# Kernel tuning notes

Hardware: AMD Instinct MI355X
Metric: run time of the kernel (lower is better)

The kernel has to match this reference:

```python
import jax, jax.numpy as jnp
import numpy as np

N_HEADS = 16  # cfg.n_heads
ROPE_BASE = 10000.0


def _rope_sin_cos(T, head_dim, dtype):
    # standard NeoX-style rotary tables, shape (T, head_dim)
    inv_freq = 1.0 / (ROPE_BASE ** (jnp.arange(0, head_dim, 2, dtype=jnp.float32) / head_dim))
    freqs = jnp.arange(T, dtype=jnp.float32)[:, None] * inv_freq[None, :]  # (T, hd/2)
    emb = jnp.concatenate([freqs, freqs], axis=-1)                          # (T, hd)
    return jnp.sin(emb).astype(dtype), jnp.cos(emb).astype(dtype)


def _rotate_half(x):
    x1, x2 = jnp.split(x, 2, axis=-1)
    return jnp.concatenate([-x2, x1], axis=-1)


def setup_inputs() -> dict:
    key = jax.random.key(0)
    kx, kq, kp, kl = jax.random.split(key, 4)
    B, T, D = 4, 2048, 2048
    x = jax.random.normal(kx, (B, T, D), dtype=jnp.float32)
    # torch Linear weights: (out_features, in_features), no bias
    Wqkv = jax.random.normal(kq, (3 * D, D), dtype=jnp.float32) * (D ** -0.5)
    Wproj = jax.random.normal(kp, (D, D), dtype=jnp.float32) * (D ** -0.5)
    # padding at the end: valid lengths in [T//2, T]
    lengths = jax.random.randint(kl, (B,), T // 2, T + 1)
    attention_mask = (jnp.arange(T)[None, :] < lengths[:, None]).astype(jnp.int32)
    return {"x": x, "Wqkv": Wqkv, "Wproj": Wproj, "attention_mask": attention_mask}


def reference(x, Wqkv, Wproj, attention_mask):
    B, T, D = x.shape
    H = N_HEADS
    hd = D // H
    qkv = (x @ Wqkv.T).reshape(B, T, 3, H, hd)            # (B,T,3,H,hd)
    q, k, v = (jnp.moveaxis(qkv[:, :, i], 1, 2) for i in range(3))  # each (B,H,T,hd)
    sin, cos = _rope_sin_cos(T, hd, x.dtype)              # (T,hd), broadcast over B,H
    q = q * cos + _rotate_half(q) * sin
    k = k * cos + _rotate_half(k) * sin
    scale = 1.0 / jnp.sqrt(jnp.asarray(hd, x.dtype))
    scores = jnp.einsum("bhqd,bhkd->bhqk", q, k) * scale  # (B,H,T,T)
    causal = jnp.triu(jnp.ones((T, T), dtype=bool), k=1)[None, None]       # (1,1,T,T)
    pad = (attention_mask == 0)[:, None, None, :]                           # (B,1,1,T)
    bias = jnp.where(causal | pad, -jnp.inf, 0.0).astype(x.dtype)
    attn = jax.nn.softmax(scores + bias, axis=-1)
    out = jnp.einsum("bhqk,bhkd->bhqd", attn, v)          # (B,H,T,hd)
    out = jnp.moveaxis(out, 1, 2).reshape(B, T, D)
    return out @ Wproj.T
```

## Files before the change

### kernel.cpp

```cpp
#include <hip/hip_runtime.h>
#include <math.h>

#define B_SZ 4
#define T_SEQ 2048
#define D_MODEL 2048
#define NH 16
#define HD 128

typedef unsigned short u16;
typedef unsigned int u32;
typedef __attribute__((ext_vector_type(8))) short short8;
typedef __attribute__((ext_vector_type(4))) float f32x4;

__device__ __forceinline__ float bf2f(u16 u) {
    return __uint_as_float(((u32)u) << 16);
}
__device__ __forceinline__ u16 f2bf(float f) {
    u32 x = __float_as_uint(f);
    return (u16)((x + 0x7fffu + ((x >> 16) & 1u)) >> 16);
}

__device__ __forceinline__ void gload_lds16(const u16* g, u16* lds) {
    __builtin_amdgcn_global_load_lds(
        (const __attribute__((address_space(1))) u32*)(const void*)g,
        (__attribute__((address_space(3))) u32*)(void*)lds, 16, 0, 0);
}

__global__ __launch_bounds__(256) void cast_kernel(const float* __restrict__ in,
                                                   u16* __restrict__ out, int n4)
{
    int idx = blockIdx.x * 256 + threadIdx.x;
    if (idx < n4) {
        float4 x = ((const float4*)in)[idx];
        ushort4 u;
        u.x = f2bf(x.x); u.y = f2bf(x.y); u.z = f2bf(x.z); u.w = f2bf(x.w);
        ((ushort4*)out)[idx] = u;
    }
}

#define TSZ 16384
#define MFMA_B16 __builtin_amdgcn_mfma_f32_16x16x32_bf16

template <int MODE>
__global__ __launch_bounds__(512, 2) void gemm256(
    const u16* __restrict__ A, const u16* __restrict__ W,
    float* __restrict__ C,
    u16* __restrict__ qb, u16* __restrict__ kb, u16* __restrict__ vb,
    int M, int N, int K)
{
    extern __shared__ u16 smem[];

    const int tid = threadIdx.x;
    const int nbx = N >> 8;
    const int nwg = gridDim.x;
    const int orig = blockIdx.x;
    const int wgid = (orig & 7) * (nwg >> 3) + (orig >> 3);
    const int bx = wgid % nbx, by = wgid / nbx;
    const int n0 = bx << 8, m0 = by << 8;

    const int w = tid >> 6, L = tid & 63;
    const int wm = w >> 2, wn = w & 3;
    const int lr = L & 15;
    const int lqb = (L >> 4) << 4;
    const int xorv = (lr & 7) << 4;
    const int cb0 = lqb ^ xorv;
    const int cb1 = (64 + lqb) ^ xorv;

    const u16* Ag = A + (size_t)m0 * K;
    const u16* Wg = W + (size_t)n0 * K;

    const int srow = tid >> 3;
    const int scb = ((tid << 4) & 127) ^ ((srow & 7) << 4);
    const size_t goff = (size_t)srow * K + (scb >> 1);
    const int loff = tid << 3;

    const int NT = K >> 6;

    f32x4 acc[8][4];
#pragma unroll
    for (int i = 0; i < 8; ++i)
#pragma unroll
        for (int j = 0; j < 4; ++j) acc[i][j] = (f32x4){0.f, 0.f, 0.f, 0.f};

#define ST_A(tt, c) gload_lds16(Ag + (size_t)((c) * 64) * K + (size_t)(tt) * 64 + goff, \
                                smem + ((tt) & 1) * TSZ + (c) * 4096 + loff)
#define ST_B(tt, c) gload_lds16(Wg + (size_t)((c) * 64) * K + (size_t)(tt) * 64 + goff, \
                                smem + 2 * TSZ + ((tt) & 1) * TSZ + (c) * 4096 + loff)

    ST_A(0, 0); ST_A(0, 2); ST_B(0, 0); ST_B(0, 1); ST_B(0, 2); ST_B(0, 3);
    ST_A(0, 1); ST_A(0, 3);
    ST_A(1, 0); ST_A(1, 2); ST_B(1, 0); ST_B(1, 1); ST_B(1, 2); ST_B(1, 3);
    asm volatile("s_waitcnt vmcnt(6)" ::: "memory");
    __builtin_amdgcn_s_barrier();

    for (int t = 0; t < NT; ++t) {
        const char* pA = (const char*)(smem + (t & 1) * TSZ) + (wm * 128 + lr) * 128;
        const char* pB = (const char*)(smem + 2 * TSZ + (t & 1) * TSZ) + (wn * 64 + lr) * 128;
        short8 alo[4][2], ahi[4][2], blo[2][2], bhi[2][2];

#pragma unroll
        for (int f = 0; f < 4; ++f) {
            alo[f][0] = *(const short8*)(pA + f * 2048 + cb0);
            alo[f][1] = *(const short8*)(pA + f * 2048 + cb1);
        }
#pragma unroll
        for (int g = 0; g < 2; ++g) {
            blo[g][0] = *(const short8*)(pB + g * 2048 + cb0);
            blo[g][1] = *(const short8*)(pB + g * 2048 + cb1);
        }
        if (t + 1 < NT) { ST_A(t + 1, 1); ST_A(t + 1, 3); }
        asm volatile("s_waitcnt lgkmcnt(8)" ::: "memory");
        __builtin_amdgcn_s_barrier();
        asm volatile("s_waitcnt lgkmcnt(0)" ::: "memory");
        __builtin_amdgcn_sched_barrier(0);
        __builtin_amdgcn_s_setprio(1);
#pragma unroll
        for (int f = 0; f < 4; ++f)
#pragma unroll
            for (int g = 0; g < 2; ++g) {
                acc[f][g] = MFMA_B16(alo[f][0], blo[g][0], acc[f][g], 0, 0, 0);
                acc[f][g] = MFMA_B16(alo[f][1], blo[g][1], acc[f][g], 0, 0, 0);
            }
        __builtin_amdgcn_s_setprio(0);
        __builtin_amdgcn_s_barrier();

#pragma unroll
        for (int g = 0; g < 2; ++g) {
            bhi[g][0] = *(const short8*)(pB + 4096 + g * 2048 + cb0);
            bhi[g][1] = *(const short8*)(pB + 4096 + g * 2048 + cb1);
        }
        if (t + 2 < NT) { ST_A(t + 2, 0); ST_A(t + 2, 2); }
        __builtin_amdgcn_s_barrier();
        asm volatile("s_waitcnt lgkmcnt(0)" ::: "memory");
        __builtin_amdgcn_sched_barrier(0);
        __builtin_amdgcn_s_setprio(1);
#pragma unroll
        for (int f = 0; f < 4; ++f)
#pragma unroll
            for (int g = 0; g < 2; ++g) {
                acc[f][2 + g] = MFMA_B16(alo[f][0], bhi[g][0], acc[f][2 + g], 0, 0, 0);
                acc[f][2 + g] = MFMA_B16(alo[f][1], bhi[g][1], acc[f][2 + g], 0, 0, 0);
            }
        __builtin_amdgcn_s_setprio(0);
        __builtin_amdgcn_s_barrier();

#pragma unroll
        for (int f = 0; f < 4; ++f) {
            ahi[f][0] = *(const short8*)(pA + 8192 + f * 2048 + cb0);
            ahi[f][1] = *(const short8*)(pA + 8192 + f * 2048 + cb1);
        }
        if (t + 2 < NT) { ST_B(t + 2, 0); ST_B(t + 2, 1); }
        __builtin_amdgcn_s_barrier();
        asm volatile("s_waitcnt lgkmcnt(0)" ::: "memory");
        __builtin_amdgcn_sched_barrier(0);
        __builtin_amdgcn_s_setprio(1);
#pragma unroll
        for (int f = 0; f < 4; ++f)
#pragma unroll
            for (int g = 0; g < 2; ++g) {
                acc[4 + f][g] = MFMA_B16(ahi[f][0], blo[g][0], acc[4 + f][g], 0, 0, 0);
                acc[4 + f][g] = MFMA_B16(ahi[f][1], blo[g][1], acc[4 + f][g], 0, 0, 0);
            }
        __builtin_amdgcn_s_setprio(0);
        __builtin_amdgcn_s_barrier();

        if (t + 2 < NT) { ST_B(t + 2, 2); ST_B(t + 2, 3); }
        if (t < NT - 2)
            asm volatile("s_waitcnt vmcnt(6)" ::: "memory");
        else
            asm volatile("s_waitcnt vmcnt(0)" ::: "memory");
        __builtin_amdgcn_s_barrier();
        __builtin_amdgcn_s_setprio(1);
#pragma unroll
        for (int f = 0; f < 4; ++f)
#pragma unroll
            for (int g = 0; g < 2; ++g) {
                acc[4 + f][2 + g] = MFMA_B16(ahi[f][0], bhi[g][0], acc[4 + f][2 + g], 0, 0, 0);
                acc[4 + f][2 + g] = MFMA_B16(ahi[f][1], bhi[g][1], acc[4 + f][2 + g], 0, 0, 0);
            }
        __builtin_amdgcn_s_setprio(0);
        __builtin_amdgcn_s_barrier();
    }
#undef ST_A
#undef ST_B

    const int lq4 = (L >> 4) << 2;

    if (MODE == 0) {
#pragma unroll
        for (int f = 0; f < 8; ++f) {
            const int m = m0 + wm * 128 + (f >> 2) * 64 + (f & 3) * 16 + lq4;
#pragma unroll
            for (int g = 0; g < 4; ++g) {
                const int n = n0 + wn * 64 + (g >> 1) * 32 + (g & 1) * 16 + lr;
#pragma unroll
                for (int r = 0; r < 4; ++r)
                    C[(size_t)(m + r) * N + n] = acc[f][g][r];
            }
        }
    } else {
        const int s = n0 >> 11;
        const int b_ = m0 >> 11;
        const int t0 = m0 & (T_SEQ - 1);
        if (s == 2) {
            u16* Ts = smem;
#pragma unroll
            for (int f = 0; f < 8; ++f) {
                const int tl = wm * 128 + (f >> 2) * 64 + (f & 3) * 16 + lq4;
#pragma unroll
                for (int g = 0; g < 4; ++g) {
                    const int c = wn * 64 + (g >> 1) * 32 + (g & 1) * 16 + lr;
                    char* rowp = (char*)Ts + c * 512;
#pragma unroll
                    for (int r = 0; r < 4; ++r)
                        *(u16*)(rowp + (((tl + r) * 2) ^ ((c & 7) << 4))) =
                            f2bf(acc[f][g][r]);
                }
            }
            __syncthreads();
            const int h0 = (n0 & 2047) >> 7;
            const int tcb = (tid & 31) << 4;
#pragma unroll
            for (int pass = 0; pass < 16; ++pass) {
                const int c = pass * 16 + (tid >> 5);
                short8 vv = *(const short8*)((const char*)Ts + c * 512 +
                                             (tcb ^ ((c & 7) << 4)));
                const int hh = c >> 7, d = c & 127;
                *(short8*)(vb + ((size_t)(b_ * NH + h0 + hh) * HD + d) * T_SEQ +
                           t0 + (tcb >> 1)) = vv;
            }
        } else {
            u16* p = (s == 0) ? qb : kb;
            const int nb = n0 & 2047;
#pragma unroll
            for (int f = 0; f < 8; ++f) {
                const int tl = t0 + wm * 128 + (f >> 2) * 64 + (f & 3) * 16 + lq4;
#pragma unroll
                for (int g = 0; g < 4; ++g) {
                    const int nn = nb + wn * 64 + (g >> 1) * 32 + (g & 1) * 16 + lr;
                    const int hh = nn >> 7, d = nn & 127;
                    u16* pb = p + ((size_t)(b_ * NH + hh) * T_SEQ + tl) * HD + d;
#pragma unroll
                    for (int r = 0; r < 4; ++r)
                        pb[(size_t)r * HD] = f2bf(acc[f][g][r]);
                }
            }
        }
    }
}

__global__ __launch_bounds__(128) void rope_kernel(u16* __restrict__ qb,
                                                   u16* __restrict__ kb)
{
    const int bht = blockIdx.x;
    const int t = bht & (T_SEQ - 1);
    const int bh = bht >> 11;
    const int tid = threadIdx.x;
    const int i = tid & 63;
    u16* buf = (tid < 64) ? qb : kb;
    const size_t base = ((size_t)bh * T_SEQ + t) * HD;

    const float inv = expf(-(2.f * (float)i / 128.f) * 9.210340371976184f);
    const float ang = (float)t * inv;
    const float s = sinf(ang);
    const float c = cosf(ang);

    const float x1 = bf2f(buf[base + i]);
    const float x2 = bf2f(buf[base + i + 64]);
    buf[base + i]      = f2bf(x1 * c - x2 * s);
    buf[base + i + 64] = f2bf(x2 * c + x1 * s);
}

__global__ __launch_bounds__(256) void attn_kernel(
    const u16* __restrict__ q, const u16* __restrict__ k,
    const u16* __restrict__ v, const int* __restrict__ mask,
    u16* __restrict__ o)
{
    __shared__ u16 QKs[4 * 64 * 32];
    __shared__ u16 Vt[2 * 128 * 32];
    __shared__ u16 Ps[4][2 * 16 * 32];

    const int tid = threadIdx.x;
    const int id = blockIdx.x;
    const int bh = id & 63;
    const int qi = 31 - (id >> 6);
    const int b = bh >> 4;
    const int q0 = qi * 64;
    const int w = tid >> 6, L = tid & 63;
    const int lr = L & 15;
    const int lq = (L >> 4) * 8;
    const float scale = 0.08838834764831845f;
    const float NEG = -1e30f;

    const u16* qg = q + (size_t)bh * T_SEQ * HD;
    const u16* kg = k + (size_t)bh * T_SEQ * HD;
    const u16* vg = v + (size_t)bh * HD * T_SEQ;
    const int* mrow = mask + b * T_SEQ;

#pragma unroll
    for (int c = 0; c < 4; ++c) {
        const int row = q0 + c * 16 + (L >> 2);
        const int col = w * 32 + (L & 3) * 8;
        gload_lds16(qg + (size_t)row * HD + col,
                    QKs + w * 2048 + c * 512 + L * 8);
    }
    __syncthreads();

    short8 qa[4];
#pragma unroll
    for (int kc = 0; kc < 4; ++kc)
        qa[kc] = *(const short8*)(QKs + kc * 2048 + (w * 16 + lr) * 32 + lq);

    f32x4 on[8];
#pragma unroll
    for (int nd = 0; nd < 8; ++nd) on[nd] = (f32x4){0.f, 0.f, 0.f, 0.f};
    float l_r[4] = {0.f, 0.f, 0.f, 0.f};

    const int row_base = q0 + w * 16 + (L >> 4) * 4;
    u16* PsW = Ps[w];

    for (int kt = 0; kt <= qi; ++kt) {
        const int kv0 = kt * 64;
        __syncthreads();
#pragma unroll
        for (int c = 0; c < 4; ++c) {
            const int row = kv0 + c * 16 + (L >> 2);
            const int col = w * 32 + (L & 3) * 8;
            gload_lds16(kg + (size_t)row * HD + col,
                        QKs + w * 2048 + c * 512 + L * 8);
        }
#pragma unroll
        for (int c = 0; c < 4; ++c) {
            const int kvc = w >> 1;
            const int dg = (w & 1) * 4 + c;
            const int d = dg * 16 + (L >> 2);
            const int t = kv0 + kvc * 32 + (L & 3) * 8;
            gload_lds16(vg + (size_t)d * T_SEQ + t,
                        Vt + kvc * 4096 + dg * 512 + L * 8);
        }
        __syncthreads();

        f32x4 sacc[4];
#pragma unroll
        for (int nt = 0; nt < 4; ++nt) {
            sacc[nt] = (f32x4){0.f, 0.f, 0.f, 0.f};
            short8 bb[4];
#pragma unroll
            for (int kc = 0; kc < 4; ++kc)
                bb[kc] = *(const short8*)(QKs + kc * 2048 + (nt * 16 + lr) * 32 + lq);
#pragma unroll
            for (int kc = 0; kc < 4; ++kc)
                sacc[nt] = __builtin_amdgcn_mfma_f32_16x16x32_bf16(
                    qa[kc], bb[kc], sacc[nt], 0, 0, 0);
        }

        const bool diag = (kt == qi);
        float ps[4][4];
#pragma unroll
        for (int nt = 0; nt < 4; ++nt) {
            const int col = kv0 + nt * 16 + lr;
            const float bias = mrow[col] ? 0.f : NEG;
#pragma unroll
            for (int r = 0; r < 4; ++r) {
                float s = sacc[nt][r] * scale + bias;
                if (diag && col > row_base + r) s = NEG;
                const float p = __expf(s);
                ps[nt][r] = p;
                l_r[r] += p;
            }
        }

#pragma unroll
        for (int nt = 0; nt < 4; ++nt) {
            const int koff = (nt & 1) * 16 + lr;
#pragma unroll
            for (int r = 0; r < 4; ++r)
                PsW[(nt >> 1) * 512 + ((L >> 4) * 4 + r) * 32 + koff] =
                    f2bf(ps[nt][r]);
        }

        short8 pa[2];
#pragma unroll
        for (int kk = 0; kk < 2; ++kk)
            pa[kk] = *(const short8*)(PsW + kk * 512 + lr * 32 + lq);
#pragma unroll
        for (int nd = 0; nd < 8; ++nd) {
            short8 vb0 = *(const short8*)(Vt + 0 * 4096 + (nd * 16 + lr) * 32 + lq);
            short8 vb1 = *(const short8*)(Vt + 1 * 4096 + (nd * 16 + lr) * 32 + lq);
            on[nd] = __builtin_amdgcn_mfma_f32_16x16x32_bf16(pa[0], vb0, on[nd], 0, 0, 0);
            on[nd] = __builtin_amdgcn_mfma_f32_16x16x32_bf16(pa[1], vb1, on[nd], 0, 0, 0);
        }
    }

#pragma unroll
    for (int off = 1; off < 16; off <<= 1)
#pragma unroll
        for (int r = 0; r < 4; ++r)
            l_r[r] += __shfl_xor(l_r[r], off);

    const int h = bh & 15;
#pragma unroll
    for (int r = 0; r < 4; ++r) {
        const float inv = 1.f / l_r[r];
        const int t = row_base + r;
        u16* op = o + ((size_t)(b * T_SEQ + t)) * D_MODEL + h * HD + lr;
#pragma unroll
        for (int nd = 0; nd < 8; ++nd)
            op[nd * 16] = f2bf(on[nd][r] * inv);
    }
}

extern "C" void kernel_launch(void* const* d_in, const int* in_sizes, int n_in,
                              void* d_out, int out_size, void* d_ws, size_t ws_size,
                              hipStream_t stream)
{
    const float* x     = (const float*)d_in[0];
    const float* Wqkv  = (const float*)d_in[1];
    const float* Wproj = (const float*)d_in[2];
    const int*   mask  = (const int*)d_in[3];
    float* out = (float*)d_out;

    const size_t E = (size_t)B_SZ * T_SEQ * D_MODEL;
    u16* xb     = (u16*)d_ws;
    u16* wqkvb  = xb + E;
    u16* wprojb = wqkvb + (size_t)3 * D_MODEL * D_MODEL;
    u16* qb     = wprojb + (size_t)D_MODEL * D_MODEL;
    u16* kb     = qb + E;
    u16* vb     = kb + E;
    u16* ob     = vb + E;

    const int M = B_SZ * T_SEQ;

    cast_kernel<<<dim3((int)(E / 4 / 256)), 256, 0, stream>>>(x, xb, (int)(E / 4));
    cast_kernel<<<dim3(3 * D_MODEL * D_MODEL / 4 / 256), 256, 0, stream>>>(
        Wqkv, wqkvb, 3 * D_MODEL * D_MODEL / 4);
    cast_kernel<<<dim3(D_MODEL * D_MODEL / 4 / 256), 256, 0, stream>>>(
        Wproj, wprojb, D_MODEL * D_MODEL / 4);

    gemm256<1><<<dim3((3 * D_MODEL / 256) * (M / 256)), 512, 131072, stream>>>(
        xb, wqkvb, nullptr, qb, kb, vb, M, 3 * D_MODEL, D_MODEL);

    rope_kernel<<<dim3(B_SZ * NH * T_SEQ), 128, 0, stream>>>(qb, kb);

    attn_kernel<<<dim3(T_SEQ / 64 * 64), 256, 0, stream>>>(qb, kb, vb, mask, ob);

    gemm256<0><<<dim3((D_MODEL / 256) * (M / 256)), 512, 131072, stream>>>(
        ob, wprojb, out, nullptr, nullptr, nullptr, M, D_MODEL, D_MODEL);
}
```

Before: 577.6 us.

## Double-buffer K/V tiles in attention with XOR-swizzled LDS and prefetch

Rewrites the attention kernel's K/V staging to use double-buffered dynamic shared memory and prefetches the next tile while computing the current one, synchronizing with vmcnt waits. LDS layouts become full-row tiles with XOR swizzling to avoid bank conflicts. It also reorders the block mapping so consecutive blocks share a head, adds s_setprio around the MFMA sections, and replaces per-column mask loads with a length computed once per block. The length shortcut assumes padding masks are contiguous at the end, and the larger LDS footprint may lower occupancy.

```diff
diff --git a/kernel.cpp b/kernel.cpp
--- a/kernel.cpp
+++ b/kernel.cpp
@@ -271,125 +271,156 @@
     buf[base + i + 64] = f2bf(x2 * c + x1 * s);
 }
 
+__device__ __forceinline__ void stage_k64(const u16* g, u16* lds, int tid) {
+#pragma unroll
+    for (int c = 0; c < 4; ++c) {
+        const int row = c * 16 + (tid >> 4);
+        const int cb = ((tid & 15) * 16) ^ ((row & 7) << 4);
+        gload_lds16(g + (size_t)row * HD + (cb >> 1), lds + c * 2048 + tid * 8);
+    }
+}
+__device__ __forceinline__ void stage_v64(const u16* g, u16* lds, int tid) {
+#pragma unroll
+    for (int c = 0; c < 4; ++c) {
+        const int row = c * 32 + (tid >> 3);
+        const int cb = ((tid & 7) * 16) ^ ((row & 7) << 4);
+        gload_lds16(g + (size_t)row * T_SEQ + (cb >> 1), lds + c * 2048 + tid * 8);
+    }
+}
+
 __global__ __launch_bounds__(256) void attn_kernel(
     const u16* __restrict__ q, const u16* __restrict__ k,
     const u16* __restrict__ v, const int* __restrict__ mask,
     u16* __restrict__ o)
 {
-    __shared__ u16 QKs[4 * 64 * 32];
-    __shared__ u16 Vt[2 * 128 * 32];
-    __shared__ u16 Ps[4][2 * 16 * 32];
+    extern __shared__ u16 smem[];
+    u16* Kb = smem;
+    u16* Vb = smem + 16384;
 
     const int tid = threadIdx.x;
     const int id = blockIdx.x;
-    const int bh = id & 63;
-    const int qi = 31 - (id >> 6);
+    const int bh = id >> 5;
+    const int qi = 31 - (id & 31);
     const int b = bh >> 4;
     const int q0 = qi * 64;
     const int w = tid >> 6, L = tid & 63;
     const int lr = L & 15;
-    const int lq = (L >> 4) * 8;
+    const int lqB = (L >> 4) * 16;
+    const int xk = (lr & 7) << 4;
     const float scale = 0.08838834764831845f;
     const float NEG = -1e30f;
+
+    char* PsW = (char*)(smem + 32768 + w * 1024);
 
     const u16* qg = q + (size_t)bh * T_SEQ * HD;
     const u16* kg = k + (size_t)bh * T_SEQ * HD;
     const u16* vg = v + (size_t)bh * HD * T_SEQ;
     const int* mrow = mask + b * T_SEQ;
 
-#pragma unroll
-    for (int c = 0; c < 4; ++c) {
-        const int row = q0 + c * 16 + (L >> 2);
-        const int col = w * 32 + (L & 3) * 8;
-        gload_lds16(qg + (size_t)row * HD + col,
-                    QKs + w * 2048 + c * 512 + L * 8);
-    }
+    stage_k64(qg + (size_t)q0 * HD, Kb, tid);
+
+    int4 ma = ((const int4*)mrow)[tid];
+    int4 mb2 = ((const int4*)mrow)[tid + 256];
+    int part = ma.x + ma.y + ma.z + ma.w + mb2.x + mb2.y + mb2.z + mb2.w;
+#pragma unroll
+    for (int off = 32; off >= 1; off >>= 1) part += __shfl_xor(part, off);
+    int* lred = (int*)(smem + 32768);
+    if (L == 0) lred[w] = part;
     __syncthreads();
+    const int len = lred[0] + lred[1] + lred[2] + lred[3];
 
     short8 qa[4];
-#pragma unroll
-    for (int kc = 0; kc < 4; ++kc)
-        qa[kc] = *(const short8*)(QKs + kc * 2048 + (w * 16 + lr) * 32 + lq);
+    {
+        const char* Kc = (const char*)Kb;
+        const int row = w * 16 + lr;
+#pragma unroll
+        for (int kc = 0; kc < 4; ++kc)
+            qa[kc] = *(const short8*)(Kc + row * 256 + ((kc * 64 + lqB) ^ xk));
+    }
+    __syncthreads();
+
+    stage_k64(kg, Kb, tid);
+    stage_v64(vg, Vb, tid);
 
     f32x4 on[8];
 #pragma unroll
     for (int nd = 0; nd < 8; ++nd) on[nd] = (f32x4){0.f, 0.f, 0.f, 0.f};
     float l_r[4] = {0.f, 0.f, 0.f, 0.f};
-
     const int row_base = q0 + w * 16 + (L >> 4) * 4;
-    u16* PsW = Ps[w];
 
     for (int kt = 0; kt <= qi; ++kt) {
         const int kv0 = kt * 64;
-        __syncthreads();
-#pragma unroll
-        for (int c = 0; c < 4; ++c) {
-            const int row = kv0 + c * 16 + (L >> 2);
-            const int col = w * 32 + (L & 3) * 8;
-            gload_lds16(kg + (size_t)row * HD + col,
-                        QKs + w * 2048 + c * 512 + L * 8);
-        }
-#pragma unroll
-        for (int c = 0; c < 4; ++c) {
-            const int kvc = w >> 1;
-            const int dg = (w & 1) * 4 + c;
-            const int d = dg * 16 + (L >> 2);
-            const int t = kv0 + kvc * 32 + (L & 3) * 8;
-            gload_lds16(vg + (size_t)d * T_SEQ + t,
-                        Vt + kvc * 4096 + dg * 512 + L * 8);
-        }
-        __syncthreads();
+        const int cur = kt & 1;
+        if (kt < qi) {
+            stage_k64(kg + (size_t)(kv0 + 64) * HD, Kb + (cur ^ 1) * 8192, tid);
+            stage_v64(vg + (kv0 + 64), Vb + (cur ^ 1) * 8192, tid);
+            asm volatile("s_waitcnt vmcnt(8)" ::: "memory");
+        } else {
+            asm volatile("s_waitcnt vmcnt(0)" ::: "memory");
+        }
+        __builtin_amdgcn_s_barrier();
+
+        const char* Kc = (const char*)(Kb + cur * 8192);
+        const char* Vc = (const char*)(Vb + cur * 8192);
 
         f32x4 sacc[4];
+        short8 bb[4][4];
+#pragma unroll
+        for (int nt = 0; nt < 4; ++nt) {
+            const char* rp = Kc + (nt * 16 + lr) * 256;
+#pragma unroll
+            for (int kc = 0; kc < 4; ++kc)
+                bb[nt][kc] = *(const short8*)(rp + ((kc * 64 + lqB) ^ xk));
+        }
+        __builtin_amdgcn_s_setprio(1);
 #pragma unroll
         for (int nt = 0; nt < 4; ++nt) {
             sacc[nt] = (f32x4){0.f, 0.f, 0.f, 0.f};
-            short8 bb[4];
 #pragma unroll
             for (int kc = 0; kc < 4; ++kc)
-                bb[kc] = *(const short8*)(QKs + kc * 2048 + (nt * 16 + lr) * 32 + lq);
-#pragma unroll
-            for (int kc = 0; kc < 4; ++kc)
-                sacc[nt] = __builtin_amdgcn_mfma_f32_16x16x32_bf16(
-                    qa[kc], bb[kc], sacc[nt], 0, 0, 0);
-        }
+                sacc[nt] = MFMA_B16(qa[kc], bb[nt][kc], sacc[nt], 0, 0, 0);
+        }
+        __builtin_amdgcn_s_setprio(0);
 
         const bool diag = (kt == qi);
-        float ps[4][4];
+        float ps_[4][4];
 #pragma unroll
         for (int nt = 0; nt < 4; ++nt) {
             const int col = kv0 + nt * 16 + lr;
-            const float bias = mrow[col] ? 0.f : NEG;
+            const float bias = (col < len) ? 0.f : NEG;
 #pragma unroll
             for (int r = 0; r < 4; ++r) {
                 float s = sacc[nt][r] * scale + bias;
                 if (diag && col > row_base + r) s = NEG;
                 const float p = __expf(s);
-                ps[nt][r] = p;
+                ps_[nt][r] = p;
                 l_r[r] += p;
             }
         }
 
 #pragma unroll
         for (int nt = 0; nt < 4; ++nt) {
-            const int koff = (nt & 1) * 16 + lr;
-#pragma unroll
-            for (int r = 0; r < 4; ++r)
-                PsW[(nt >> 1) * 512 + ((L >> 4) * 4 + r) * 32 + koff] =
-                    f2bf(ps[nt][r]);
-        }
-
-        short8 pa[2];
-#pragma unroll
-        for (int kk = 0; kk < 2; ++kk)
-            pa[kk] = *(const short8*)(PsW + kk * 512 + lr * 32 + lq);
+#pragma unroll
+            for (int r = 0; r < 4; ++r) {
+                const int pr = (L >> 4) * 4 + r;
+                *(u16*)(PsW + pr * 128 + (((nt * 16 + lr) * 2) ^ ((pr & 7) << 4))) =
+                    f2bf(ps_[nt][r]);
+            }
+        }
+
+        short8 pa0 = *(const short8*)(PsW + lr * 128 + (lqB ^ xk));
+        short8 pa1 = *(const short8*)(PsW + lr * 128 + ((64 + lqB) ^ xk));
+        __builtin_amdgcn_s_setprio(1);
 #pragma unroll
         for (int nd = 0; nd < 8; ++nd) {
-            short8 vb0 = *(const short8*)(Vt + 0 * 4096 + (nd * 16 + lr) * 32 + lq);
-            short8 vb1 = *(const short8*)(Vt + 1 * 4096 + (nd * 16 + lr) * 32 + lq);
-            on[nd] = __builtin_amdgcn_mfma_f32_16x16x32_bf16(pa[0], vb0, on[nd], 0, 0, 0);
-            on[nd] = __builtin_amdgcn_mfma_f32_16x16x32_bf16(pa[1], vb1, on[nd], 0, 0, 0);
-        }
+            const char* vp = Vc + (nd * 16 + lr) * 128;
+            short8 vb0 = *(const short8*)(vp + (lqB ^ xk));
+            short8 vb1 = *(const short8*)(vp + ((64 + lqB) ^ xk));
+            on[nd] = MFMA_B16(pa0, vb0, on[nd], 0, 0, 0);
+            on[nd] = MFMA_B16(pa1, vb1, on[nd], 0, 0, 0);
+        }
+        __builtin_amdgcn_s_setprio(0);
+        __builtin_amdgcn_s_barrier();
     }
 
 #pragma unroll
@@ -442,7 +473,7 @@
 
     rope_kernel<<<dim3(B_SZ * NH * T_SEQ), 128, 0, stream>>>(qb, kb);
 
-    attn_kernel<<<dim3(T_SEQ / 64 * 64), 256, 0, stream>>>(qb, kb, vb, mask, ob);
+    attn_kernel<<<dim3(T_SEQ / 64 * 64), 256, 73728, stream>>>(qb, kb, vb, mask, ob);
 
     gemm256<0><<<dim3((D_MODEL / 256) * (M / 256)), 512, 131072, stream>>>(
         ob, wprojb, out, nullptr, nullptr, nullptr, M, D_MODEL, D_MODEL);
```

After: 661.2 us. 1.14x slower.
